# Kernel optimization log

Measured on AMD Instinct MI355X. Metric: run time of the kernel, lower is better.

Reference implementation:

```python
import jax, jax.numpy as jnp
import numpy as np
import math

D_MODEL = 1024
EXPAND = 2
D_INNER = EXPAND * D_MODEL  # 2048
D_STATE = 16
D_CONV = 4
DT_RANK = math.ceil(D_MODEL / 16)  # 64
BATCH = 1
SEQLEN = 2048


def _silu(x):
    return x * jax.nn.sigmoid(x)


def _selective_scan(u, delta, A, B, C, D, z, delta_bias):
    """u, delta, z: (b,d,l); A: (d,n); B, C: (b,n,l); D, delta_bias: (d)."""
    delta = jax.nn.softplus(delta + delta_bias[None, :, None])        # (b,d,l)
    dA = jnp.exp(jnp.einsum('bdl,dn->lbdn', delta, A))                # (l,b,d,n)
    dBu = jnp.einsum('bdl,bnl->lbdn', delta * u, B)                   # (l,b,d,n)
    Ct = jnp.transpose(C, (2, 0, 1))                                  # (l,b,n)

    def step(h, inp):
        dA_t, dBu_t, C_t = inp
        h = dA_t * h + dBu_t                                          # (b,d,n)
        y = jnp.einsum('bdn,bn->bd', h, C_t)
        return h, y

    h0 = jnp.zeros((u.shape[0], u.shape[1], A.shape[1]), dtype=u.dtype)
    _, ys = jax.lax.scan(step, h0, (dA, dBu, Ct))                     # ys: (l,b,d)
    y = jnp.transpose(ys, (1, 2, 0))                                  # (b,d,l)
    y = y + D[:, None] * u
    return y * _silu(z)


def _causal_conv1d(x, conv_w, conv_b):
    """x: (b,d,l); conv_w: (d,w); conv_b: (d). Depthwise causal conv."""
    x_pad = jnp.pad(x, ((0, 0), (0, 0), (D_CONV - 1, 0)))
    kernel = conv_w[:, None, :]  # (d, 1, w)
    y = jax.lax.conv_general_dilated(
        x_pad, kernel, window_strides=(1,), padding='VALID',
        dimension_numbers=('NCH', 'OIH', 'NCH'),
        feature_group_count=D_INNER)
    return y + conv_b[None, :, None]


def setup_inputs() -> dict:
    key = jax.random.key(0)
    ks = jax.random.split(key, 12)
    hidden_states = jax.random.normal(ks[0], (BATCH, SEQLEN, D_MODEL), dtype=jnp.float32)
    in_proj_w = jax.random.normal(ks[1], (2 * D_INNER, D_MODEL), dtype=jnp.float32) * (D_MODEL ** -0.5)
    conv_w = jax.random.normal(ks[2], (D_INNER, D_CONV), dtype=jnp.float32) * (D_CONV ** -0.5)
    conv_b = jnp.zeros((D_INNER,), dtype=jnp.float32)
    dt_std = DT_RANK ** -0.5

    def dt_bias(k):
        dt = jnp.exp(jax.random.uniform(k, (D_INNER,)) * (math.log(0.1) - math.log(0.001)) + math.log(0.001))
        dt = jnp.clip(dt, 1e-4, None)
        return dt + jnp.log(-jnp.expm1(-dt))  # inverse softplus

    A_log = jnp.log(jnp.broadcast_to(jnp.arange(1, D_STATE + 1, dtype=jnp.float32), (D_INNER, D_STATE)))
    x1_proj_w = jax.random.normal(ks[3], (DT_RANK + 2 * D_STATE, D_INNER), dtype=jnp.float32) * (D_INNER ** -0.5)
    dt1_proj_w = jax.random.uniform(ks[4], (D_INNER, DT_RANK), minval=-dt_std, maxval=dt_std)
    dt1_proj_b = dt_bias(ks[5])
    x2_proj_w = jax.random.normal(ks[6], (DT_RANK + 2 * D_STATE, D_INNER), dtype=jnp.float32) * (D_INNER ** -0.5)
    dt2_proj_w = jax.random.uniform(ks[7], (D_INNER, DT_RANK), minval=-dt_std, maxval=dt_std)
    dt2_proj_b = dt_bias(ks[8])
    out_proj_w = jax.random.normal(ks[9], (D_MODEL, D_INNER), dtype=jnp.float32) * (D_INNER ** -0.5)
    return {
        'hidden_states': hidden_states,
        'in_proj_w': in_proj_w, 'conv_w': conv_w, 'conv_b': conv_b,
        'x1_proj_w': x1_proj_w, 'dt1_proj_w': dt1_proj_w, 'dt1_proj_b': dt1_proj_b,
        'A1_log': A_log, 'D1': jnp.ones((D_INNER,), dtype=jnp.float32),
        'x2_proj_w': x2_proj_w, 'dt2_proj_w': dt2_proj_w, 'dt2_proj_b': dt2_proj_b,
        'A2_log': A_log, 'D2': jnp.ones((D_INNER,), dtype=jnp.float32),
        'out_proj_w': out_proj_w,
    }


def reference(hidden_states, in_proj_w, conv_w, conv_b,
              x1_proj_w, dt1_proj_w, dt1_proj_b, A1_log, D1,
              x2_proj_w, dt2_proj_w, dt2_proj_b, A2_log, D2,
              out_proj_w):
    # in_proj: (b,l,d) @ W^T -> (b, 2*d_inner, l)
    xz = jnp.einsum('bld,ed->bel', hidden_states, in_proj_w)
    x, z = jnp.split(xz, 2, axis=1)                                   # (b,d_inner,l) each
    A1 = -jnp.exp(A1_log.astype(jnp.float32))
    A2 = -jnp.exp(A2_log.astype(jnp.float32))
    x = _silu(_causal_conv1d(x, conv_w, conv_b))                      # (b,d_inner,l)

    def branch_params(xp_w, dtp_w):
        dbl = jnp.einsum('bdl,kd->bkl', x, xp_w)                      # (b, r+2n, l)
        dt, Bm, Cm = jnp.split(dbl, [DT_RANK, DT_RANK + D_STATE], axis=1)
        dt = jnp.einsum('brl,dr->bdl', dt, dtp_w)
        return dt, Bm, Cm

    dt1, B1, C1 = branch_params(x1_proj_w, dt1_proj_w)
    dt2, B2, C2 = branch_params(x2_proj_w, dt2_proj_w)
    y1 = _selective_scan(x, dt1, A1, B1, C1, D1.astype(jnp.float32), z, dt1_proj_b.astype(jnp.float32))
    y2 = _selective_scan(x, dt2, A2, B2, C2, D2.astype(jnp.float32), z, dt2_proj_b.astype(jnp.float32))
    y = y1 - y2                                                       # (b,d_inner,l)
    out = jnp.einsum('bdl,od->blo', y, out_proj_w)                    # (b,l,d_model)
    return out
```

## Files before the change

### kernel.cpp

```cpp
#include <hip/hip_runtime.h>
#include <math.h>

#define SEQ 2048
#define DMODEL 1024
#define DIN 2048
#define NST 16
#define DTR 64
#define CH 32
#define NCH (SEQ / CH)
#define LOG2E 1.4426950408889634f

typedef __attribute__((ext_vector_type(8))) _Float16 f16x8;
typedef __attribute__((ext_vector_type(4))) float f32x4;

__device__ __forceinline__ ushort f2h(float f) {
  union { _Float16 h; ushort u; } c; c.h = (_Float16)f; return c.u;
}
__device__ __forceinline__ float h2f(ushort u) {
  union { ushort u; _Float16 h; } c; c.u = u; return (float)c.h;
}
__device__ __forceinline__ ushort2 split2(float v) {
  ushort hh = f2h(v);
  return make_ushort2(hh, f2h((v - h2f(hh)) * 2048.f));
}
__device__ __forceinline__ float join2(ushort2 p) {
  return h2f(p.x) + h2f(p.y) * (1.f / 2048.f);
}
__device__ __forceinline__ float splus(float v) {
  return v > 20.f ? v : log1pf(__expf(v));
}
__device__ __forceinline__ void powers16(float e, float* p) {
  float e2 = e * e, e4 = e2 * e2, e8 = e4 * e4;
  p[0] = e;       p[1] = e2;       p[2] = e2 * e;   p[3] = e4;
  p[4] = e4 * e;  p[5] = e4 * e2;  p[6] = e4 * p[2]; p[7] = e8;
  p[8] = e8 * e;  p[9] = e8 * e2;  p[10] = e8 * p[2]; p[11] = e8 * e4;
  p[12] = e8 * p[4]; p[13] = e8 * p[5]; p[14] = e8 * p[6]; p[15] = e8 * e8;
}

#define GLL(g, l) __builtin_amdgcn_global_load_lds( \
    (const __attribute__((address_space(1))) void*)(g), \
    (__attribute__((address_space(3))) void*)(l), 16, 0, 0)

#define XCD_SWZ(BMv, BNv)                                              \
  const int nwg_ = gridDim.x * gridDim.y;                              \
  const int flat_ = blockIdx.y * gridDim.x + blockIdx.x;               \
  const int swz_ = (flat_ & 7) * (nwg_ >> 3) + (flat_ >> 3);           \
  const int m0 = (swz_ / gridDim.x) * (BMv);                           \
  const int n0 = (swz_ % gridDim.x) * (BNv);

template<int BM, int BN, int SPLITK, int MODE>
__global__ __launch_bounds__(256, 2) void gemm3p(const ushort* __restrict__ Ahi,
                                                 const ushort* __restrict__ Alo,
                                                 const ushort* __restrict__ Bhi,
                                                 const ushort* __restrict__ Blo,
                                                 float* __restrict__ C,
                                                 int M, int N, int K) {
  constexpr int WM = BM / 2, WN = BN / 2, TM = WM / 16, TN = WN / 16;
  constexpr int SA = BM / 16, SB = BN / 16;
  constexpr bool dropB = (MODE == 2);
  __shared__ __align__(16) ushort sAh[2][BM * 32], sAl[2][BM * 32];
  __shared__ __align__(16) ushort sBh[2][BN * 32];
  __shared__ __align__(16) ushort sBl[2][dropB ? 16 : BN * 32];
  const int tid = threadIdx.x, wid = tid >> 6, lane = tid & 63;
  XCD_SWZ(BM, BN)
  const int Kc = K / SPLITK, kbeg = blockIdx.z * Kc;
  const int wm0 = (wid >> 1) * WM, wn0 = (wid & 1) * WN;
  const int fr = lane & 15;
  const int lrow = lane >> 2;
  const int lkc = (lane & 3) ^ ((lane >> 3) & 3);
  const int fpo = fr * 32 + (((lane >> 4) ^ ((lane >> 1) & 3)) * 8);

  f32x4 acc[TM][TN], accL[TM][TN];
#pragma unroll
  for (int mi = 0; mi < TM; ++mi)
#pragma unroll
    for (int ni = 0; ni < TN; ++ni)
#pragma unroll
      for (int r = 0; r < 4; ++r) { acc[mi][ni][r] = 0.f; accL[mi][ni][r] = 0.f; }

  for (int k0 = 0; k0 < Kc; k0 += 64) {
    __syncthreads();
#pragma unroll
    for (int kk = 0; kk < 2; ++kk) {
      const int kg = kbeg + k0 + kk * 32 + lkc * 8;
#pragma unroll
      for (int i = 0; i < SA / 4; ++i) {
        const int seg = wid * (SA / 4) + i;
        const size_t ga = (size_t)(m0 + seg * 16 + lrow) * K + kg;
        GLL(&Ahi[ga], &sAh[kk][seg * 512]);
        GLL(&Alo[ga], &sAl[kk][seg * 512]);
      }
#pragma unroll
      for (int i = 0; i < SB / 4; ++i) {
        const int seg = wid * (SB / 4) + i;
        const size_t ga = (size_t)(n0 + seg * 16 + lrow) * K + kg;
        GLL(&Bhi[ga], &sBh[kk][seg * 512]);
        if constexpr (!dropB) GLL(&Blo[ga], &sBl[kk][seg * 512]);
      }
    }
    __syncthreads();

#pragma unroll
    for (int kk = 0; kk < 2; ++kk) {
      f16x8 ah[TM], al[TM], bh[TN], bl[TN];
#pragma unroll
      for (int mi = 0; mi < TM; ++mi) {
        const int r = (wm0 / 16 + mi) * 512 + fpo;
        ah[mi] = *(const f16x8*)&sAh[kk][r];
        al[mi] = *(const f16x8*)&sAl[kk][r];
      }
#pragma unroll
      for (int ni = 0; ni < TN; ++ni) {
        const int r = (wn0 / 16 + ni) * 512 + fpo;
        bh[ni] = *(const f16x8*)&sBh[kk][r];
        if constexpr (!dropB) bl[ni] = *(const f16x8*)&sBl[kk][r];
      }
#pragma unroll
      for (int mi = 0; mi < TM; ++mi)
#pragma unroll
        for (int ni = 0; ni < TN; ++ni) {
          acc[mi][ni] = __builtin_amdgcn_mfma_f32_16x16x32_f16(ah[mi], bh[ni], acc[mi][ni], 0, 0, 0);
          accL[mi][ni] = __builtin_amdgcn_mfma_f32_16x16x32_f16(al[mi], bh[ni], accL[mi][ni], 0, 0, 0);
          if constexpr (!dropB)
            accL[mi][ni] = __builtin_amdgcn_mfma_f32_16x16x32_f16(ah[mi], bl[ni], accL[mi][ni], 0, 0, 0);
        }
    }
  }

  float* __restrict__ Co = C + (size_t)blockIdx.z * M * N;
#pragma unroll
  for (int mi = 0; mi < TM; ++mi)
#pragma unroll
    for (int ni = 0; ni < TN; ++ni)
#pragma unroll
      for (int r = 0; r < 4; ++r)
        Co[(size_t)(m0 + wm0 + mi * 16 + (lane >> 4) * 4 + r) * N + n0 + wn0 + ni * 16 + fr] =
            acc[mi][ni][r] + accL[mi][ni][r] * (1.f / 2048.f);
}

__global__ __launch_bounds__(256, 2) void dt_mfma(const ushort* __restrict__ dtT_hi,
                                                  const ushort* __restrict__ dtT_lo,
                                                  const ushort* __restrict__ dw_hi,
                                                  const ushort* __restrict__ dw_lo,
                                                  const float* __restrict__ b1,
                                                  const float* __restrict__ b2,
                                                  ushort2* __restrict__ sp1,
                                                  ushort2* __restrict__ sp2) {
  const int br = blockIdx.z;
  const ushort* __restrict__ Ah = dtT_hi + (size_t)br * 131072;
  const ushort* __restrict__ Al_ = dtT_lo + (size_t)br * 131072;
  const ushort* __restrict__ Bh = dw_hi + (size_t)br * 131072;
  const ushort* __restrict__ Bl = dw_lo + (size_t)br * 131072;
  const float* __restrict__ bias = br ? b2 : b1;
  ushort2* __restrict__ o = br ? sp2 : sp1;
  __shared__ __align__(16) ushort sAh[2][4096], sAl[2][4096];
  __shared__ __align__(16) ushort sBh[2][4096], sBl[2][4096];
  const int tid = threadIdx.x, wid = tid >> 6, lane = tid & 63;
  XCD_SWZ(128, 128)
  const int wm0 = (wid >> 1) * 64, wn0 = (wid & 1) * 64;
  const int fr = lane & 15;
  const int lrow = lane >> 2;
  const int lkc = (lane & 3) ^ ((lane >> 3) & 3);
  const int fpo = fr * 32 + (((lane >> 4) ^ ((lane >> 1) & 3)) * 8);

  f32x4 acc[4][4], accL[4][4];
#pragma unroll
  for (int mi = 0; mi < 4; ++mi)
#pragma unroll
    for (int ni = 0; ni < 4; ++ni)
#pragma unroll
      for (int r = 0; r < 4; ++r) { acc[mi][ni][r] = 0.f; accL[mi][ni][r] = 0.f; }

#pragma unroll
  for (int kk = 0; kk < 2; ++kk) {
    const int kg = kk * 32 + lkc * 8;
#pragma unroll
    for (int i = 0; i < 2; ++i) {
      const int seg = wid * 2 + i;
      const size_t ga = (size_t)(m0 + seg * 16 + lrow) * 64 + kg;
      GLL(&Ah[ga], &sAh[kk][seg * 512]);
      GLL(&Al_[ga], &sAl[kk][seg * 512]);
      const size_t gb = (size_t)(n0 + seg * 16 + lrow) * 64 + kg;
      GLL(&Bh[gb], &sBh[kk][seg * 512]);
      GLL(&Bl[gb], &sBl[kk][seg * 512]);
    }
  }
  __syncthreads();

#pragma unroll
  for (int kk = 0; kk < 2; ++kk) {
    f16x8 ah[4], al[4], bh[4], bl[4];
#pragma unroll
    for (int mi = 0; mi < 4; ++mi) {
      const int r = (wm0 / 16 + mi) * 512 + fpo;
      ah[mi] = *(const f16x8*)&sAh[kk][r];
      al[mi] = *(const f16x8*)&sAl[kk][r];
    }
#pragma unroll
    for (int ni = 0; ni < 4; ++ni) {
      const int r = (wn0 / 16 + ni) * 512 + fpo;
      bh[ni] = *(const f16x8*)&sBh[kk][r];
      bl[ni] = *(const f16x8*)&sBl[kk][r];
    }
#pragma unroll
    for (int mi = 0; mi < 4; ++mi)
#pragma unroll
      for (int ni = 0; ni < 4; ++ni) {
        acc[mi][ni] = __builtin_amdgcn_mfma_f32_16x16x32_f16(ah[mi], bh[ni], acc[mi][ni], 0, 0, 0);
        accL[mi][ni] = __builtin_amdgcn_mfma_f32_16x16x32_f16(al[mi], bh[ni], accL[mi][ni], 0, 0, 0);
        accL[mi][ni] = __builtin_amdgcn_mfma_f32_16x16x32_f16(ah[mi], bl[ni], accL[mi][ni], 0, 0, 0);
      }
  }

#pragma unroll
  for (int ni = 0; ni < 4; ++ni) {
    const int n = n0 + wn0 + ni * 16 + fr;
    const float bv = bias[n];
#pragma unroll
    for (int mi = 0; mi < 4; ++mi)
#pragma unroll
      for (int r = 0; r < 4; ++r) {
        const int m = m0 + wm0 + mi * 16 + (lane >> 4) * 4 + r;
        const float v = splus(acc[mi][ni][r] + accL[mi][ni][r] * (1.f / 2048.f) + bv);
        o[(size_t)m * DIN + n] = split2(v);
      }
  }
}

__device__ __forceinline__ void split_store4h(float4 v, ushort* hi, ushort* lo, size_t i) {
  ushort h0 = f2h(v.x), h1 = f2h(v.y), h2 = f2h(v.z), h3 = f2h(v.w);
  *(ushort4*)&hi[i] = make_ushort4(h0, h1, h2, h3);
  *(ushort4*)&lo[i] = make_ushort4(f2h((v.x - h2f(h0)) * 2048.f), f2h((v.y - h2f(h1)) * 2048.f),
                                   f2h((v.z - h2f(h2)) * 2048.f), f2h((v.w - h2f(h3)) * 2048.f));
}

__global__ __launch_bounds__(256) void cvt_fused(const float* __restrict__ inw,
                                                 const float* __restrict__ hid,
                                                 const float* __restrict__ x1w,
                                                 const float* __restrict__ x2w,
                                                 const float* __restrict__ dtw1,
                                                 const float* __restrict__ dtw2,
                                                 ushort* __restrict__ w_hi, ushort* __restrict__ w_lo,
                                                 ushort* __restrict__ h_hi,
                                                 ushort* __restrict__ wx_hi, ushort* __restrict__ wx_lo,
                                                 ushort* __restrict__ dw_hi, ushort* __restrict__ dw_lo) {
  const int q = blockIdx.x * 256 + threadIdx.x;
  if (q >= 1048576 && q < 1572864) {
    const size_t i = (size_t)(q - 1048576) * 4;
    float4 v = *(const float4*)&hid[i];
    *(ushort4*)&h_hi[i] = make_ushort4(f2h(v.x), f2h(v.y), f2h(v.z), f2h(v.w));
    return;
  }
  const float* src; ushort* dhi; ushort* dlo; int base;
  if (q < 1048576)       { src = inw; dhi = w_hi;  dlo = w_lo;  base = q; }
  else if (q < 1622016)  { src = x1w; dhi = wx_hi; dlo = wx_lo; base = q - 1572864; }
  else if (q < 1671168)  { src = x2w; dhi = wx_hi + 196608; dlo = wx_lo + 196608; base = q - 1622016; }
  else if (q < 1703936)  { src = dtw1; dhi = dw_hi; dlo = dw_lo; base = q - 1671168; }
  else                   { src = dtw2; dhi = dw_hi + 131072; dlo = dw_lo + 131072; base = q - 1703936; }
  const size_t i = (size_t)base * 4;
  split_store4h(*(const float4*)&src[i], dhi, dlo, i);
}

__global__ __launch_bounds__(256) void reduce_out(const float* __restrict__ p,
                                                  float* __restrict__ o, int n) {
  const int i = (blockIdx.x * 256 + threadIdx.x) * 4;
  if (i >= n) return;
  float4 a = *(const float4*)&p[i];
  float4 b = *(const float4*)&p[(size_t)n + i];
  float4 c = *(const float4*)&p[(size_t)2 * n + i];
  float4 d = *(const float4*)&p[(size_t)3 * n + i];
  *(float4*)&o[i] = make_float4(a.x + b.x + c.x + d.x, a.y + b.y + c.y + d.y,
                                a.z + b.z + c.z + d.z, a.w + b.w + c.w + d.w);
}

__global__ __launch_bounds__(256) void conv_tr_kernel(const float* __restrict__ xz,
                                                      const float* __restrict__ cw,
                                                      const float* __restrict__ cb,
                                                      ushort* __restrict__ xcT_hi,
                                                      ushort* __restrict__ xcT_lo,
                                                      ushort2* __restrict__ zs) {
  const int l0 = blockIdx.x * 64, d0 = blockIdx.y * 64;
  const int tid = threadIdx.x;
  __shared__ float xin[64][68];
  __shared__ float To[64][65];
  __shared__ float cwS[64][4];
  __shared__ float cbS[64];

  for (int i = tid; i < 1024; i += 256) {
    const int d = i >> 4, q = i & 15;
    float4 v = *(const float4*)&xz[(size_t)(d0 + d) * SEQ + l0 + q * 4];
    xin[d][3 + q * 4 + 0] = v.x; xin[d][3 + q * 4 + 1] = v.y;
    xin[d][3 + q * 4 + 2] = v.z; xin[d][3 + q * 4 + 3] = v.w;
  }
  if (tid < 192) {
    const int j = tid >> 6, d = tid & 63;
    const int l = l0 - 3 + j;
    xin[d][j] = (l >= 0) ? xz[(size_t)(d0 + d) * SEQ + l] : 0.f;
  }
  if (tid < 64) {
    cbS[tid] = cb[d0 + tid];
    float4 w = *(const float4*)&cw[(d0 + tid) * 4];
    cwS[tid][0] = w.x; cwS[tid][1] = w.y; cwS[tid][2] = w.z; cwS[tid][3] = w.w;
  }
  __syncthreads();

  for (int i = tid; i < 4096; i += 256) {
    const int d = i >> 6, l = i & 63;
    float a = cbS[d] + cwS[d][0] * xin[d][l] + cwS[d][1] * xin[d][l + 1] +
              cwS[d][2] * xin[d][l + 2] + cwS[d][3] * xin[d][l + 3];
    To[d][l] = a / (1.f + __expf(-a));
  }
  __syncthreads();

  for (int i = tid; i < 4096; i += 256) {
    const int l = i >> 6, dd = i & 63;
    float v = To[dd][l];
    ushort h = f2h(v);
    xcT_hi[(size_t)(l0 + l) * DIN + d0 + dd] = h;
    xcT_lo[(size_t)(l0 + l) * DIN + d0 + dd] = f2h((v - h2f(h)) * 2048.f);
  }
  __syncthreads();

  for (int i = tid; i < 1024; i += 256) {
    const int d = i >> 4, q = i & 15;
    float4 v = *(const float4*)&xz[(size_t)(DIN + d0 + d) * SEQ + l0 + q * 4];
    To[d][q * 4 + 0] = v.x / (1.f + __expf(-v.x));
    To[d][q * 4 + 1] = v.y / (1.f + __expf(-v.y));
    To[d][q * 4 + 2] = v.z / (1.f + __expf(-v.z));
    To[d][q * 4 + 3] = v.w / (1.f + __expf(-v.w));
  }
  __syncthreads();
  for (int i = tid; i < 4096; i += 256) {
    const int l = i >> 6, dd = i & 63;
    zs[(size_t)(l0 + l) * DIN + d0 + dd] = split2(To[dd][l]);
  }
}

__global__ __launch_bounds__(256) void reduce_dblT_kernel(const float* __restrict__ p,
                                                          float* __restrict__ BT1,
                                                          float* __restrict__ CT1,
                                                          float* __restrict__ BT2,
                                                          float* __restrict__ CT2,
                                                          ushort* __restrict__ dtT_hi,
                                                          ushort* __restrict__ dtT_lo) {
  const int NE = SEQ * 192;
  const int idx = blockIdx.x * 256 + threadIdx.x;
  float s = 0.f;
#pragma unroll
  for (int cc = 0; cc < 16; ++cc) s += p[(size_t)cc * NE + idx];
  const int l = idx / 192, k = idx - l * 192;
  if (k < 64) {
    const size_t off = (size_t)l * 64 + k;
    const ushort hh = f2h(s);
    dtT_hi[off] = hh; dtT_lo[off] = f2h((s - h2f(hh)) * 2048.f);
  } else if (k < 80)  BT1[l * NST + (k - 64)] = s;
  else if (k < 96)    CT1[l * NST + (k - 80)] = s;
  else if (k < 160) {
    const size_t off = 131072 + (size_t)l * 64 + (k - 96);
    const ushort hh = f2h(s);
    dtT_hi[off] = hh; dtT_lo[off] = f2h((s - h2f(hh)) * 2048.f);
  }
  else if (k < 176)   BT2[l * NST + (k - 160)] = s;
  else                CT2[l * NST + (k - 176)] = s;
}

__global__ __launch_bounds__(256) void scan_phase_a(const ushort* __restrict__ uhi,
                                                    const ushort* __restrict__ ulo,
                                                    const ushort2* __restrict__ sp1,
                                                    const ushort2* __restrict__ sp2,
                                                    const float* __restrict__ BT1,
                                                    const float* __restrict__ BT2,
                                                    const float* __restrict__ Al1,
                                                    const float* __restrict__ Al2,
                                                    float* __restrict__ hend,
                                                    float* __restrict__ Pend) {
  const int c = blockIdx.y, t0 = c * CH;
  const int d = blockIdx.x * 256 + threadIdx.x;
  const size_t gbase = (size_t)t0 * DIN + d;

  __shared__ __align__(16) float Bs[2][CH][NST];
  {
    const int j = threadIdx.x;
    if (j < 128) ((float4*)&Bs[0][0][0])[j] = ((const float4*)&BT1[(size_t)t0 * NST])[j];
    else ((float4*)&Bs[1][0][0])[j - 128] = ((const float4*)&BT2[(size_t)t0 * NST])[j - 128];
  }
  __syncthreads();

  bool fast = true;
#pragma unroll
  for (int n = 0; n < NST; ++n) {
    float k1 = __expf(Al1[(size_t)d * NST + n]);
    float k2 = __expf(Al2[(size_t)d * NST + n]);
    fast = fast && (fabsf(k1 - (float)(n + 1)) < 1e-3f) && (fabsf(k2 - (float)(n + 1)) < 1e-3f);
  }
  float h1[NST], h2[NST];
#pragma unroll
  for (int n = 0; n < NST; ++n) { h1[n] = 0.f; h2[n] = 0.f; }
  float S1 = 0.f, S2 = 0.f;

  if (fast) {
    for (int tt = 0; tt < CH / 4; ++tt) {
      float s1[4], s2[4], ua[4];
#pragma unroll
      for (int j = 0; j < 4; ++j) {
        const size_t idx = gbase + (size_t)(tt * 4 + j) * DIN;
        s1[j] = join2(sp1[idx]);
        s2[j] = join2(sp2[idx]);
        ua[j] = h2f(uhi[idx]) + h2f(ulo[idx]) * (1.f / 2048.f);
      }
#pragma unroll
      for (int j = 0; j < 4; ++j) {
        const int t = tt * 4 + j;
        S1 += s1[j]; S2 += s2[j];
        const float spu1 = s1[j] * ua[j], spu2 = s2[j] * ua[j];
        float p[NST];
        powers16(__expf(-s1[j]), p);
#pragma unroll
        for (int n = 0; n < NST; ++n) h1[n] = fmaf(p[n], h1[n], spu1 * Bs[0][t][n]);
        powers16(__expf(-s2[j]), p);
#pragma unroll
        for (int n = 0; n < NST; ++n) h2[n] = fmaf(p[n], h2[n], spu2 * Bs[1][t][n]);
      }
    }
  } else {
    float A1e[NST], A2e[NST];
#pragma unroll
    for (int n = 0; n < NST; ++n) {
      A1e[n] = -__expf(Al1[(size_t)d * NST + n]) * LOG2E;
      A2e[n] = -__expf(Al2[(size_t)d * NST + n]) * LOG2E;
    }
    for (int tt = 0; tt < CH / 4; ++tt) {
      float s1[4], s2[4], ua[4];
#pragma unroll
      for (int j = 0; j < 4; ++j) {
        const size_t idx = gbase + (size_t)(tt * 4 + j) * DIN;
        s1[j] = join2(sp1[idx]);
        s2[j] = join2(sp2[idx]);
        ua[j] = h2f(uhi[idx]) + h2f(ulo[idx]) * (1.f / 2048.f);
      }
#pragma unroll
      for (int j = 0; j < 4; ++j) {
        const int t = tt * 4 + j;
        S1 += s1[j]; S2 += s2[j];
        const float spu1 = s1[j] * ua[j], spu2 = s2[j] * ua[j];
#pragma unroll
        for (int n = 0; n < NST; ++n) {
          h1[n] = fmaf(exp2f(A1e[n] * s1[j]), h1[n], spu1 * Bs[0][t][n]);
          h2[n] = fmaf(exp2f(A2e[n] * s2[j]), h2[n], spu2 * Bs[1][t][n]);
        }
      }
    }
  }

  float P1[NST], P2[NST];
  if (fast) {
    powers16(__expf(-S1), P1);
    powers16(__expf(-S2), P2);
  } else {
#pragma unroll
    for (int n = 0; n < NST; ++n) {
      P1[n] = exp2f(-__expf(Al1[(size_t)d * NST + n]) * LOG2E * S1);
      P2[n] = exp2f(-__expf(Al2[(size_t)d * NST + n]) * LOG2E * S2);
    }
  }
  const size_t b1 = ((size_t)c * DIN + d) * NST;
  const size_t b2 = ((size_t)(NCH + c) * DIN + d) * NST;
#pragma unroll
  for (int n = 0; n < NST; n += 4) {
    *(float4*)&hend[b1 + n] = make_float4(h1[n], h1[n + 1], h1[n + 2], h1[n + 3]);
    *(float4*)&Pend[b1 + n] = make_float4(P1[n], P1[n + 1], P1[n + 2], P1[n + 3]);
    *(float4*)&hend[b2 + n] = make_float4(h2[n], h2[n + 1], h2[n + 2], h2[n + 3]);
    *(float4*)&Pend[b2 + n] = make_float4(P2[n], P2[n + 1], P2[n + 2], P2[n + 3]);
  }
}

__global__ __launch_bounds__(256) void carry_cvt(const float* __restrict__ hend,
                                                 float* __restrict__ PendHin,
                                                 const float* __restrict__ outw,
                                                 ushort* __restrict__ ow_hi) {
  const int b = blockIdx.x;
  if (b < 256) {
    const int flat = b * 256 + threadIdx.x;
    const int br = flat >> 15;
    const int dn = flat & 32767;
    float h = 0.f;
    for (int c = 0; c < NCH; ++c) {
      size_t idx = ((size_t)(br * NCH + c) << 15) + dn;
      float Pv = PendHin[idx];
      float he = hend[idx];
      PendHin[idx] = h;
      h = fmaf(Pv, h, he);
    }
  } else {
    const size_t i = ((size_t)(b - 256) * 256 + threadIdx.x) * 4;
    float4 v = *(const float4*)&outw[i];
    *(ushort4*)&ow_hi[i] = make_ushort4(f2h(v.x), f2h(v.y), f2h(v.z), f2h(v.w));
  }
}

__global__ __launch_bounds__(256) void scan_phase_c(const ushort* __restrict__ uhi,
                                                    const ushort* __restrict__ ulo,
                                                    const ushort2* __restrict__ sp1,
                                                    const ushort2* __restrict__ sp2,
                                                    const float* __restrict__ BT1,
                                                    const float* __restrict__ CT1,
                                                    const float* __restrict__ BT2,
                                                    const float* __restrict__ CT2,
                                                    const float* __restrict__ Al1,
                                                    const float* __restrict__ Al2,
                                                    const float* __restrict__ D1,
                                                    const float* __restrict__ D2,
                                                    const float* __restrict__ hin,
                                                    const ushort2* __restrict__ zs,
                                                    ushort* __restrict__ yd_hi,
                                                    ushort* __restrict__ yd_lo) {
  const int c = blockIdx.y, t0 = c * CH;
  const int d = blockIdx.x * 256 + threadIdx.x;
  const size_t gbase = (size_t)t0 * DIN + d;

  __shared__ __align__(16) float Bs[2][CH][NST];
  __shared__ __align__(16) float Cs[2][CH][NST];
  {
    const int j = threadIdx.x;
    if (j < 128) {
      ((float4*)&Bs[0][0][0])[j] = ((const float4*)&BT1[(size_t)t0 * NST])[j];
      ((float4*)&Cs[0][0][0])[j] = ((const float4*)&CT1[(size_t)t0 * NST])[j];
    } else {
      ((float4*)&Bs[1][0][0])[j - 128] = ((const float4*)&BT2[(size_t)t0 * NST])[j - 128];
      ((float4*)&Cs[1][0][0])[j - 128] = ((const float4*)&CT2[(size_t)t0 * NST])[j - 128];
    }
  }
  __syncthreads();

  bool fast = true;
#pragma unroll
  for (int n = 0; n < NST; ++n) {
    float k1 = __expf(Al1[(size_t)d * NST + n]);
    float k2 = __expf(Al2[(size_t)d * NST + n]);
    fast = fast && (fabsf(k1 - (float)(n + 1)) < 1e-3f) && (fabsf(k2 - (float)(n + 1)) < 1e-3f);
  }
  const float Ddd = D1[d] - D2[d];
  float h1[NST], h2[NST];
  const size_t hb1 = ((size_t)c * DIN + d) * NST;
  const size_t hb2 = ((size_t)(NCH + c) * DIN + d) * NST;
#pragma unroll
  for (int n = 0; n < NST; n += 4) {
    float4 v1 = *(const float4*)&hin[hb1 + n];
    h1[n] = v1.x; h1[n + 1] = v1.y; h1[n + 2] = v1.z; h1[n + 3] = v1.w;
    float4 v2 = *(const float4*)&hin[hb2 + n];
    h2[n] = v2.x; h2[n + 1] = v2.y; h2[n + 2] = v2.z; h2[n + 3] = v2.w;
  }

  if (fast) {
    for (int tt = 0; tt < CH / 4; ++tt) {
      float s1[4], s2[4], ua[4];
#pragma unroll
      for (int j = 0; j < 4; ++j) {
        const size_t idx = gbase + (size_t)(tt * 4 + j) * DIN;
        s1[j] = join2(sp1[idx]);
        s2[j] = join2(sp2[idx]);
        ua[j] = h2f(uhi[idx]) + h2f(ulo[idx]) * (1.f / 2048.f);
      }
#pragma unroll
      for (int j = 0; j < 4; ++j) {
        const int t = tt * 4 + j;
        const size_t idx = gbase + (size_t)t * DIN;
        const float spu1 = s1[j] * ua[j], spu2 = s2[j] * ua[j];
        float p[NST];
        float y1 = 0.f, y2 = 0.f;
        powers16(__expf(-s1[j]), p);
#pragma unroll
        for (int n = 0; n < NST; ++n) {
          h1[n] = fmaf(p[n], h1[n], spu1 * Bs[0][t][n]);
          y1 = fmaf(h1[n], Cs[0][t][n], y1);
        }
        powers16(__expf(-s2[j]), p);
#pragma unroll
        for (int n = 0; n < NST; ++n) {
          h2[n] = fmaf(p[n], h2[n], spu2 * Bs[1][t][n]);
          y2 = fmaf(h2[n], Cs[1][t][n], y2);
        }
        const float zv = join2(zs[idx]);
        const float yd = (y1 - y2 + Ddd * ua[j]) * zv;
        const ushort hh = f2h(yd);
        yd_hi[idx] = hh;
        yd_lo[idx] = f2h((yd - h2f(hh)) * 2048.f);
      }
    }
  } else {
    float A1e[NST], A2e[NST];
#pragma unroll
    for (int n = 0; n < NST; ++n) {
      A1e[n] = -__expf(Al1[(size_t)d * NST + n]) * LOG2E;
      A2e[n] = -__expf(Al2[(size_t)d * NST + n]) * LOG2E;
    }
    for (int tt = 0; tt < CH / 4; ++tt) {
      float s1[4], s2[4], ua[4];
#pragma unroll
      for (int j = 0; j < 4; ++j) {
        const size_t idx = gbase + (size_t)(tt * 4 + j) * DIN;
        s1[j] = join2(sp1[idx]);
        s2[j] = join2(sp2[idx]);
        ua[j] = h2f(uhi[idx]) + h2f(ulo[idx]) * (1.f / 2048.f);
      }
#pragma unroll
      for (int j = 0; j < 4; ++j) {
        const int t = tt * 4 + j;
        const size_t idx = gbase + (size_t)t * DIN;
        const float spu1 = s1[j] * ua[j], spu2 = s2[j] * ua[j];
        float y1 = 0.f, y2 = 0.f;
#pragma unroll
        for (int n = 0; n < NST; ++n) {
          h1[n] = fmaf(exp2f(A1e[n] * s1[j]), h1[n], spu1 * Bs[0][t][n]);
          y1 = fmaf(h1[n], Cs[0][t][n], y1);
          h2[n] = fmaf(exp2f(A2e[n] * s2[j]), h2[n], spu2 * Bs[1][t][n]);
          y2 = fmaf(h2[n], Cs[1][t][n], y2);
        }
        const float zv = join2(zs[idx]);
        const float yd = (y1 - y2 + Ddd * ua[j]) * zv;
        const ushort hh = f2h(yd);
        yd_hi[idx] = hh;
        yd_lo[idx] = f2h((yd - h2f(hh)) * 2048.f);
      }
    }
  }
}

extern "C" void kernel_launch(void* const* d_in, const int* in_sizes, int n_in,
                              void* d_out, int out_size, void* d_ws, size_t ws_size,
                              hipStream_t stream) {
  const float* hidden = (const float*)d_in[0];
  const float* in_proj_w = (const float*)d_in[1];
  const float* conv_w = (const float*)d_in[2];
  const float* conv_b = (const float*)d_in[3];
  const float* x1w = (const float*)d_in[4];
  const float* dtw1 = (const float*)d_in[5];
  const float* dtb1 = (const float*)d_in[6];
  const float* Al1 = (const float*)d_in[7];
  const float* D1 = (const float*)d_in[8];
  const float* x2w = (const float*)d_in[9];
  const float* dtw2 = (const float*)d_in[10];
  const float* dtb2 = (const float*)d_in[11];
  const float* Al2 = (const float*)d_in[12];
  const float* D2 = (const float*)d_in[13];
  const float* outw = (const float*)d_in[14];
  float* out = (float*)d_out;

  float* ws = (float*)d_ws;
  float* xz = ws;
  float* xcTbuf = xz + (size_t)4096 * SEQ;
  float* dtTbuf = xcTbuf + (size_t)SEQ * DIN;
  float* spbuf1 = dtTbuf + (size_t)192 * SEQ;
  float* spbuf2 = spbuf1 + (size_t)SEQ * DIN;
  float* zsbuf = spbuf2 + (size_t)SEQ * DIN;
  float* hendB = zsbuf + (size_t)SEQ * DIN;
  float* PendB = hendB + (size_t)2 * NCH * DIN * NST;
  float* BT1 = PendB + (size_t)2 * NCH * DIN * NST;
  float* CT1 = BT1 + (size_t)SEQ * NST;
  float* BT2 = CT1 + (size_t)SEQ * NST;
  float* CT2 = BT2 + (size_t)SEQ * NST;
  float* wxp = CT2 + (size_t)SEQ * NST;

  ushort* xcT_hi = (ushort*)xcTbuf;
  ushort* xcT_lo = (ushort*)(xcTbuf + 2097152);
  ushort* dtT_hi = (ushort*)dtTbuf;
  ushort* dtT_lo = dtT_hi + 262144;
  ushort2* sp1 = (ushort2*)spbuf1;
  ushort2* sp2 = (ushort2*)spbuf2;
  ushort2* zs = (ushort2*)zsbuf;
  ushort* w_hi = (ushort*)zsbuf;
  ushort* w_lo = (ushort*)(zsbuf + 2097152);
  ushort* h_hi = (ushort*)hendB;
  ushort* dw_hi = ((ushort*)hendB) + 2097152;
  ushort* dw_lo = dw_hi + 262144;
  ushort* wx_hi = (ushort*)wxp;
  ushort* wx_lo = (ushort*)(wxp + 196608);
  float* xp_part = spbuf1;
  ushort* yd_hi = (ushort*)xcTbuf;
  ushort* yd_lo = (ushort*)(xcTbuf + 2097152);
  ushort* ow_hi = (ushort*)xz;
  float* opart = spbuf1;
  dim3 blk(256);

  cvt_fused<<<dim3(6784), blk, 0, stream>>>(in_proj_w, hidden, x1w, x2w, dtw1, dtw2,
                                            w_hi, w_lo, h_hi, wx_hi, wx_lo, dw_hi, dw_lo);

  gemm3p<128, 128, 1, 2><<<dim3(SEQ / 128, 4096 / 128, 1), blk, 0, stream>>>(
      w_hi, w_lo, h_hi, h_hi, xz, 4096, SEQ, DMODEL);

  conv_tr_kernel<<<dim3(SEQ / 64, DIN / 64), blk, 0, stream>>>(
      xz, conv_w, conv_b, xcT_hi, xcT_lo, zs);

  gemm3p<128, 64, 16, 0><<<dim3(192 / 64, SEQ / 128, 16), blk, 0, stream>>>(
      xcT_hi, xcT_lo, wx_hi, wx_lo, xp_part, SEQ, 192, DIN);

  reduce_dblT_kernel<<<dim3(192 * SEQ / 256), blk, 0, stream>>>(
      xp_part, BT1, CT1, BT2, CT2, dtT_hi, dtT_lo);

  dt_mfma<<<dim3(DIN / 128, SEQ / 128, 2), blk, 0, stream>>>(
      dtT_hi, dtT_lo, dw_hi, dw_lo, dtb1, dtb2, sp1, sp2);

  scan_phase_a<<<dim3(DIN / 256, NCH), blk, 0, stream>>>(
      xcT_hi, xcT_lo, sp1, sp2, BT1, BT2, Al1, Al2, hendB, PendB);
  carry_cvt<<<dim3(2304), blk, 0, stream>>>(hendB, PendB, outw, ow_hi);
  scan_phase_c<<<dim3(DIN / 256, NCH), blk, 0, stream>>>(
      xcT_hi, xcT_lo, sp1, sp2, BT1, CT1, BT2, CT2, Al1, Al2,
      D1, D2, PendB, zs, yd_hi, yd_lo);

  gemm3p<128, 128, 4, 2><<<dim3(DMODEL / 128, SEQ / 128, 4), blk, 0, stream>>>(
      yd_hi, yd_lo, ow_hi, ow_hi, opart, SEQ, DMODEL, DIN);
  reduce_out<<<dim3(SEQ * DMODEL / 1024), blk, 0, stream>>>(opart, out, SEQ * DMODEL);
}
```

Measured before the change: 316.8 us.

## Double-buffer GEMM K-loop staging and prefetch carry loads in carry_cvt

```diff
diff --git a/kernel.cpp b/kernel.cpp
--- a/kernel.cpp
+++ b/kernel.cpp
@@ -55,12 +55,13 @@
                                                  const ushort* __restrict__ Blo,
                                                  float* __restrict__ C,
                                                  int M, int N, int K) {
+  constexpr int BK = 32;
   constexpr int WM = BM / 2, WN = BN / 2, TM = WM / 16, TN = WN / 16;
   constexpr int SA = BM / 16, SB = BN / 16;
   constexpr bool dropB = (MODE == 2);
-  __shared__ __align__(16) ushort sAh[2][BM * 32], sAl[2][BM * 32];
-  __shared__ __align__(16) ushort sBh[2][BN * 32];
-  __shared__ __align__(16) ushort sBl[2][dropB ? 16 : BN * 32];
+  __shared__ __align__(16) ushort sAh[2][BM * BK], sAl[2][BM * BK];
+  __shared__ __align__(16) ushort sBh[2][BN * BK];
+  __shared__ __align__(16) ushort sBl[2][dropB ? 16 : BN * BK];
   const int tid = threadIdx.x, wid = tid >> 6, lane = tid & 63;
   XCD_SWZ(BM, BN)
   const int Kc = K / SPLITK, kbeg = blockIdx.z * Kc;
@@ -78,54 +79,61 @@
 #pragma unroll
       for (int r = 0; r < 4; ++r) { acc[mi][ni][r] = 0.f; accL[mi][ni][r] = 0.f; }
 
-  for (int k0 = 0; k0 < Kc; k0 += 64) {
+#define STG(BUF, K0) do {                                                  \
+    const int kg_ = kbeg + (K0) + lkc * 8;                                 \
+    _Pragma("unroll")                                                      \
+    for (int i_ = 0; i_ < SA / 4; ++i_) {                                  \
+      const int seg_ = wid * (SA / 4) + i_;                                \
+      const size_t ga_ = (size_t)(m0 + seg_ * 16 + lrow) * K + kg_;        \
+      GLL(&Ahi[ga_], &sAh[BUF][seg_ * 512]);                               \
+      GLL(&Alo[ga_], &sAl[BUF][seg_ * 512]);                               \
+    }                                                                      \
+    _Pragma("unroll")                                                      \
+    for (int i_ = 0; i_ < SB / 4; ++i_) {                                  \
+      const int seg_ = wid * (SB / 4) + i_;                                \
+      const size_t gb_ = (size_t)(n0 + seg_ * 16 + lrow) * K + kg_;        \
+      GLL(&Bhi[gb_], &sBh[BUF][seg_ * 512]);                               \
+      if constexpr (!dropB) GLL(&Blo[gb_], &sBl[BUF][seg_ * 512]);         \
+    }                                                                      \
+  } while (0)
+
+#define CMP(BUF) do {                                                      \
+    f16x8 ah_[TM], al_[TM], bh_[TN], bl_[TN];                              \
+    _Pragma("unroll")                                                      \
+    for (int mi = 0; mi < TM; ++mi) {                                      \
+      const int r_ = (wm0 / 16 + mi) * 512 + fpo;                          \
+      ah_[mi] = *(const f16x8*)&sAh[BUF][r_];                              \
+      al_[mi] = *(const f16x8*)&sAl[BUF][r_];                              \
+    }                                                                      \
+    _Pragma("unroll")                                                      \
+    for (int ni = 0; ni < TN; ++ni) {                                      \
+      const int r_ = (wn0 / 16 + ni) * 512 + fpo;                          \
+      bh_[ni] = *(const f16x8*)&sBh[BUF][r_];                              \
+      if constexpr (!dropB) bl_[ni] = *(const f16x8*)&sBl[BUF][r_];        \
+    }                                                                      \
+    _Pragma("unroll")                                                      \
+    for (int mi = 0; mi < TM; ++mi)                                        \
+      _Pragma("unroll")                                                    \
+      for (int ni = 0; ni < TN; ++ni) {                                    \
+        acc[mi][ni] = __builtin_amdgcn_mfma_f32_16x16x32_f16(ah_[mi], bh_[ni], acc[mi][ni], 0, 0, 0);   \
+        accL[mi][ni] = __builtin_amdgcn_mfma_f32_16x16x32_f16(al_[mi], bh_[ni], accL[mi][ni], 0, 0, 0); \
+        if constexpr (!dropB)                                              \
+          accL[mi][ni] = __builtin_amdgcn_mfma_f32_16x16x32_f16(ah_[mi], bl_[ni], accL[mi][ni], 0, 0, 0); \
+      }                                                                    \
+  } while (0)
+
+  STG(0, 0);
+  __syncthreads();
+  for (int k0 = 0; k0 < Kc; k0 += 2 * BK) {
+    if (k0 + BK < Kc) STG(1, k0 + BK);
+    CMP(0);
     __syncthreads();
-#pragma unroll
-    for (int kk = 0; kk < 2; ++kk) {
-      const int kg = kbeg + k0 + kk * 32 + lkc * 8;
-#pragma unroll
-      for (int i = 0; i < SA / 4; ++i) {
-        const int seg = wid * (SA / 4) + i;
-        const size_t ga = (size_t)(m0 + seg * 16 + lrow) * K + kg;
-        GLL(&Ahi[ga], &sAh[kk][seg * 512]);
-        GLL(&Alo[ga], &sAl[kk][seg * 512]);
-      }
-#pragma unroll
-      for (int i = 0; i < SB / 4; ++i) {
-        const int seg = wid * (SB / 4) + i;
-        const size_t ga = (size_t)(n0 + seg * 16 + lrow) * K + kg;
-        GLL(&Bhi[ga], &sBh[kk][seg * 512]);
-        if constexpr (!dropB) GLL(&Blo[ga], &sBl[kk][seg * 512]);
-      }
-    }
+    if (k0 + 2 * BK < Kc) STG(0, k0 + 2 * BK);
+    if (k0 + BK < Kc) CMP(1);
     __syncthreads();
-
-#pragma unroll
-    for (int kk = 0; kk < 2; ++kk) {
-      f16x8 ah[TM], al[TM], bh[TN], bl[TN];
-#pragma unroll
-      for (int mi = 0; mi < TM; ++mi) {
-        const int r = (wm0 / 16 + mi) * 512 + fpo;
-        ah[mi] = *(const f16x8*)&sAh[kk][r];
-        al[mi] = *(const f16x8*)&sAl[kk][r];
-      }
-#pragma unroll
-      for (int ni = 0; ni < TN; ++ni) {
-        const int r = (wn0 / 16 + ni) * 512 + fpo;
-        bh[ni] = *(const f16x8*)&sBh[kk][r];
-        if constexpr (!dropB) bl[ni] = *(const f16x8*)&sBl[kk][r];
-      }
-#pragma unroll
-      for (int mi = 0; mi < TM; ++mi)
-#pragma unroll
-        for (int ni = 0; ni < TN; ++ni) {
-          acc[mi][ni] = __builtin_amdgcn_mfma_f32_16x16x32_f16(ah[mi], bh[ni], acc[mi][ni], 0, 0, 0);
-          accL[mi][ni] = __builtin_amdgcn_mfma_f32_16x16x32_f16(al[mi], bh[ni], accL[mi][ni], 0, 0, 0);
-          if constexpr (!dropB)
-            accL[mi][ni] = __builtin_amdgcn_mfma_f32_16x16x32_f16(ah[mi], bl[ni], accL[mi][ni], 0, 0, 0);
-        }
-    }
-  }
+  }
+#undef STG
+#undef CMP
 
   float* __restrict__ Co = C + (size_t)blockIdx.z * M * N;
 #pragma unroll
@@ -483,13 +491,17 @@
     const int flat = b * 256 + threadIdx.x;
     const int br = flat >> 15;
     const int dn = flat & 32767;
+    size_t idx = ((size_t)(br * NCH) << 15) + dn;
     float h = 0.f;
+    float Pv = PendHin[idx];
+    float he = hend[idx];
     for (int c = 0; c < NCH; ++c) {
-      size_t idx = ((size_t)(br * NCH + c) << 15) + dn;
-      float Pv = PendHin[idx];
-      float he = hend[idx];
+      const size_t nidx = idx + (1u << 15);
+      float Pn = 0.f, hn = 0.f;
+      if (c + 1 < NCH) { Pn = PendHin[nidx]; hn = hend[nidx]; }
       PendHin[idx] = h;
       h = fmaf(Pv, h, he);
+      Pv = Pn; he = hn; idx = nidx;
     }
   } else {
     const size_t i = ((size_t)(b - 256) * 256 + threadIdx.x) * 4;
```

Result: slower. 324.5 us (+2.4%).

## Fuse dt projection and softplus into both scan phases via per-block MFMA tiles

Applied to the files above, without the earlier changes.

```diff
diff --git a/kernel.cpp b/kernel.cpp
--- a/kernel.cpp
+++ b/kernel.cpp
@@ -138,92 +138,64 @@
             acc[mi][ni][r] + accL[mi][ni][r] * (1.f / 2048.f);
 }
 
-__global__ __launch_bounds__(256, 2) void dt_mfma(const ushort* __restrict__ dtT_hi,
-                                                  const ushort* __restrict__ dtT_lo,
-                                                  const ushort* __restrict__ dw_hi,
-                                                  const ushort* __restrict__ dw_lo,
-                                                  const float* __restrict__ b1,
-                                                  const float* __restrict__ b2,
-                                                  ushort2* __restrict__ sp1,
-                                                  ushort2* __restrict__ sp2) {
-  const int br = blockIdx.z;
-  const ushort* __restrict__ Ah = dtT_hi + (size_t)br * 131072;
-  const ushort* __restrict__ Al_ = dtT_lo + (size_t)br * 131072;
-  const ushort* __restrict__ Bh = dw_hi + (size_t)br * 131072;
-  const ushort* __restrict__ Bl = dw_lo + (size_t)br * 131072;
-  const float* __restrict__ bias = br ? b2 : b1;
-  ushort2* __restrict__ o = br ? sp2 : sp1;
-  __shared__ __align__(16) ushort sAh[2][4096], sAl[2][4096];
-  __shared__ __align__(16) ushort sBh[2][4096], sBl[2][4096];
-  const int tid = threadIdx.x, wid = tid >> 6, lane = tid & 63;
-  XCD_SWZ(128, 128)
-  const int wm0 = (wid >> 1) * 64, wn0 = (wid & 1) * 64;
-  const int fr = lane & 15;
-  const int lrow = lane >> 2;
-  const int lkc = (lane & 3) ^ ((lane >> 3) & 3);
-  const int fpo = fr * 32 + (((lane >> 4) ^ ((lane >> 1) & 3)) * 8);
-
-  f32x4 acc[4][4], accL[4][4];
-#pragma unroll
-  for (int mi = 0; mi < 4; ++mi)
-#pragma unroll
-    for (int ni = 0; ni < 4; ++ni)
-#pragma unroll
-      for (int r = 0; r < 4; ++r) { acc[mi][ni][r] = 0.f; accL[mi][ni][r] = 0.f; }
-
-#pragma unroll
-  for (int kk = 0; kk < 2; ++kk) {
-    const int kg = kk * 32 + lkc * 8;
-#pragma unroll
-    for (int i = 0; i < 2; ++i) {
-      const int seg = wid * 2 + i;
-      const size_t ga = (size_t)(m0 + seg * 16 + lrow) * 64 + kg;
-      GLL(&Ah[ga], &sAh[kk][seg * 512]);
-      GLL(&Al_[ga], &sAl[kk][seg * 512]);
-      const size_t gb = (size_t)(n0 + seg * 16 + lrow) * 64 + kg;
-      GLL(&Bh[gb], &sBh[kk][seg * 512]);
-      GLL(&Bl[gb], &sBl[kk][seg * 512]);
-    }
-  }
-  __syncthreads();
-
-#pragma unroll
-  for (int kk = 0; kk < 2; ++kk) {
-    f16x8 ah[4], al[4], bh[4], bl[4];
-#pragma unroll
-    for (int mi = 0; mi < 4; ++mi) {
-      const int r = (wm0 / 16 + mi) * 512 + fpo;
-      ah[mi] = *(const f16x8*)&sAh[kk][r];
-      al[mi] = *(const f16x8*)&sAl[kk][r];
+__device__ __forceinline__ void dt_tile(const ushort* __restrict__ dtT_hi,
+                                        const ushort* __restrict__ dtT_lo,
+                                        const ushort* __restrict__ dw_hi,
+                                        const ushort* __restrict__ dw_lo,
+                                        const float* __restrict__ b1,
+                                        const float* __restrict__ b2,
+                                        int t0, int d0, int tid,
+                                        float (*sp_s)[CH][260]) {
+  const int wid = tid >> 6, lane = tid & 63;
+  const int fr = lane & 15, kq = lane >> 4;
+#pragma unroll
+  for (int br = 0; br < 2; ++br) {
+    const ushort* __restrict__ Ah = dtT_hi + br * 131072;
+    const ushort* __restrict__ Al = dtT_lo + br * 131072;
+    const ushort* __restrict__ Bh = dw_hi + br * 131072;
+    const ushort* __restrict__ Bl = dw_lo + br * 131072;
+    const float* __restrict__ bias = br ? b2 : b1;
+    f32x4 acc[2][4], accL[2][4];
+#pragma unroll
+    for (int mi = 0; mi < 2; ++mi)
+#pragma unroll
+      for (int ni = 0; ni < 4; ++ni)
+#pragma unroll
+        for (int r = 0; r < 4; ++r) { acc[mi][ni][r] = 0.f; accL[mi][ni][r] = 0.f; }
+#pragma unroll
+    for (int kk = 0; kk < 2; ++kk) {
+      f16x8 a_h[2], a_l[2], b_h[4], b_l[4];
+#pragma unroll
+      for (int mi = 0; mi < 2; ++mi) {
+        const size_t off = (size_t)(t0 + mi * 16 + fr) * 64 + kk * 32 + kq * 8;
+        a_h[mi] = *(const f16x8*)&Ah[off];
+        a_l[mi] = *(const f16x8*)&Al[off];
+      }
+#pragma unroll
+      for (int ni = 0; ni < 4; ++ni) {
+        const size_t off = (size_t)(d0 + wid * 64 + ni * 16 + fr) * 64 + kk * 32 + kq * 8;
+        b_h[ni] = *(const f16x8*)&Bh[off];
+        b_l[ni] = *(const f16x8*)&Bl[off];
+      }
+#pragma unroll
+      for (int mi = 0; mi < 2; ++mi)
+#pragma unroll
+        for (int ni = 0; ni < 4; ++ni) {
+          acc[mi][ni] = __builtin_amdgcn_mfma_f32_16x16x32_f16(a_h[mi], b_h[ni], acc[mi][ni], 0, 0, 0);
+          accL[mi][ni] = __builtin_amdgcn_mfma_f32_16x16x32_f16(a_l[mi], b_h[ni], accL[mi][ni], 0, 0, 0);
+          accL[mi][ni] = __builtin_amdgcn_mfma_f32_16x16x32_f16(a_h[mi], b_l[ni], accL[mi][ni], 0, 0, 0);
+        }
     }
 #pragma unroll
     for (int ni = 0; ni < 4; ++ni) {
-      const int r = (wn0 / 16 + ni) * 512 + fpo;
-      bh[ni] = *(const f16x8*)&sBh[kk][r];
-      bl[ni] = *(const f16x8*)&sBl[kk][r];
-    }
-#pragma unroll
-    for (int mi = 0; mi < 4; ++mi)
-#pragma unroll
-      for (int ni = 0; ni < 4; ++ni) {
-        acc[mi][ni] = __builtin_amdgcn_mfma_f32_16x16x32_f16(ah[mi], bh[ni], acc[mi][ni], 0, 0, 0);
-        accL[mi][ni] = __builtin_amdgcn_mfma_f32_16x16x32_f16(al[mi], bh[ni], accL[mi][ni], 0, 0, 0);
-        accL[mi][ni] = __builtin_amdgcn_mfma_f32_16x16x32_f16(ah[mi], bl[ni], accL[mi][ni], 0, 0, 0);
-      }
-  }
-
-#pragma unroll
-  for (int ni = 0; ni < 4; ++ni) {
-    const int n = n0 + wn0 + ni * 16 + fr;
-    const float bv = bias[n];
-#pragma unroll
-    for (int mi = 0; mi < 4; ++mi)
-#pragma unroll
-      for (int r = 0; r < 4; ++r) {
-        const int m = m0 + wm0 + mi * 16 + (lane >> 4) * 4 + r;
-        const float v = splus(acc[mi][ni][r] + accL[mi][ni][r] * (1.f / 2048.f) + bv);
-        o[(size_t)m * DIN + n] = split2(v);
-      }
+      const float bv = bias[d0 + wid * 64 + ni * 16 + fr];
+#pragma unroll
+      for (int mi = 0; mi < 2; ++mi)
+#pragma unroll
+        for (int r = 0; r < 4; ++r)
+          sp_s[br][mi * 16 + kq * 4 + r][wid * 64 + ni * 16 + fr] =
+              splus(acc[mi][ni][r] + accL[mi][ni][r] * (1.f / 2048.f) + bv);
+    }
   }
 }
 
@@ -366,8 +338,12 @@
 
 __global__ __launch_bounds__(256) void scan_phase_a(const ushort* __restrict__ uhi,
                                                     const ushort* __restrict__ ulo,
-                                                    const ushort2* __restrict__ sp1,
-                                                    const ushort2* __restrict__ sp2,
+                                                    const ushort* __restrict__ dtT_hi,
+                                                    const ushort* __restrict__ dtT_lo,
+                                                    const ushort* __restrict__ dw_hi,
+                                                    const ushort* __restrict__ dw_lo,
+                                                    const float* __restrict__ dtb1,
+                                                    const float* __restrict__ dtb2,
                                                     const float* __restrict__ BT1,
                                                     const float* __restrict__ BT2,
                                                     const float* __restrict__ Al1,
@@ -375,15 +351,18 @@
                                                     float* __restrict__ hend,
                                                     float* __restrict__ Pend) {
   const int c = blockIdx.y, t0 = c * CH;
-  const int d = blockIdx.x * 256 + threadIdx.x;
+  const int d0b = blockIdx.x * 256;
+  const int d = d0b + threadIdx.x;
   const size_t gbase = (size_t)t0 * DIN + d;
 
   __shared__ __align__(16) float Bs[2][CH][NST];
+  __shared__ __align__(16) float sp_s[2][CH][260];
   {
     const int j = threadIdx.x;
     if (j < 128) ((float4*)&Bs[0][0][0])[j] = ((const float4*)&BT1[(size_t)t0 * NST])[j];
     else ((float4*)&Bs[1][0][0])[j - 128] = ((const float4*)&BT2[(size_t)t0 * NST])[j - 128];
   }
+  dt_tile(dtT_hi, dtT_lo, dw_hi, dw_lo, dtb1, dtb2, t0, d0b, threadIdx.x, sp_s);
   __syncthreads();
 
   bool fast = true;
@@ -404,8 +383,8 @@
 #pragma unroll
       for (int j = 0; j < 4; ++j) {
         const size_t idx = gbase + (size_t)(tt * 4 + j) * DIN;
-        s1[j] = join2(sp1[idx]);
-        s2[j] = join2(sp2[idx]);
+        s1[j] = sp_s[0][tt * 4 + j][threadIdx.x];
+        s2[j] = sp_s[1][tt * 4 + j][threadIdx.x];
         ua[j] = h2f(uhi[idx]) + h2f(ulo[idx]) * (1.f / 2048.f);
       }
 #pragma unroll
@@ -434,8 +413,8 @@
 #pragma unroll
       for (int j = 0; j < 4; ++j) {
         const size_t idx = gbase + (size_t)(tt * 4 + j) * DIN;
-        s1[j] = join2(sp1[idx]);
-        s2[j] = join2(sp2[idx]);
+        s1[j] = sp_s[0][tt * 4 + j][threadIdx.x];
+        s2[j] = sp_s[1][tt * 4 + j][threadIdx.x];
         ua[j] = h2f(uhi[idx]) + h2f(ulo[idx]) * (1.f / 2048.f);
       }
 #pragma unroll
@@ -500,8 +479,12 @@
 
 __global__ __launch_bounds__(256) void scan_phase_c(const ushort* __restrict__ uhi,
                                                     const ushort* __restrict__ ulo,
-                                                    const ushort2* __restrict__ sp1,
-                                                    const ushort2* __restrict__ sp2,
+                                                    const ushort* __restrict__ dtT_hi,
+                                                    const ushort* __restrict__ dtT_lo,
+                                                    const ushort* __restrict__ dw_hi,
+                                                    const ushort* __restrict__ dw_lo,
+                                                    const float* __restrict__ dtb1,
+                                                    const float* __restrict__ dtb2,
                                                     const float* __restrict__ BT1,
                                                     const float* __restrict__ CT1,
                                                     const float* __restrict__ BT2,
@@ -515,11 +498,13 @@
                                                     ushort* __restrict__ yd_hi,
                                                     ushort* __restrict__ yd_lo) {
   const int c = blockIdx.y, t0 = c * CH;
-  const int d = blockIdx.x * 256 + threadIdx.x;
+  const int d0b = blockIdx.x * 256;
+  const int d = d0b + threadIdx.x;
   const size_t gbase = (size_t)t0 * DIN + d;
 
   __shared__ __align__(16) float Bs[2][CH][NST];
   __shared__ __align__(16) float Cs[2][CH][NST];
+  __shared__ __align__(16) float sp_s[2][CH][260];
   {
     const int j = threadIdx.x;
     if (j < 128) {
@@ -530,6 +515,7 @@
       ((float4*)&Cs[1][0][0])[j - 128] = ((const float4*)&CT2[(size_t)t0 * NST])[j - 128];
     }
   }
+  dt_tile(dtT_hi, dtT_lo, dw_hi, dw_lo, dtb1, dtb2, t0, d0b, threadIdx.x, sp_s);
   __syncthreads();
 
   bool fast = true;
@@ -557,8 +543,8 @@
 #pragma unroll
       for (int j = 0; j < 4; ++j) {
         const size_t idx = gbase + (size_t)(tt * 4 + j) * DIN;
-        s1[j] = join2(sp1[idx]);
-        s2[j] = join2(sp2[idx]);
+        s1[j] = sp_s[0][tt * 4 + j][threadIdx.x];
+        s2[j] = sp_s[1][tt * 4 + j][threadIdx.x];
         ua[j] = h2f(uhi[idx]) + h2f(ulo[idx]) * (1.f / 2048.f);
       }
 #pragma unroll
@@ -599,8 +585,8 @@
 #pragma unroll
       for (int j = 0; j < 4; ++j) {
         const size_t idx = gbase + (size_t)(tt * 4 + j) * DIN;
-        s1[j] = join2(sp1[idx]);
-        s2[j] = join2(sp2[idx]);
+        s1[j] = sp_s[0][tt * 4 + j][threadIdx.x];
+        s2[j] = sp_s[1][tt * 4 + j][threadIdx.x];
         ua[j] = h2f(uhi[idx]) + h2f(ulo[idx]) * (1.f / 2048.f);
       }
 #pragma unroll
@@ -665,13 +651,11 @@
   ushort* xcT_lo = (ushort*)(xcTbuf + 2097152);
   ushort* dtT_hi = (ushort*)dtTbuf;
   ushort* dtT_lo = dtT_hi + 262144;
-  ushort2* sp1 = (ushort2*)spbuf1;
-  ushort2* sp2 = (ushort2*)spbuf2;
   ushort2* zs = (ushort2*)zsbuf;
   ushort* w_hi = (ushort*)zsbuf;
   ushort* w_lo = (ushort*)(zsbuf + 2097152);
   ushort* h_hi = (ushort*)hendB;
-  ushort* dw_hi = ((ushort*)hendB) + 2097152;
+  ushort* dw_hi = (ushort*)(spbuf2 + 3932160);
   ushort* dw_lo = dw_hi + 262144;
   ushort* wx_hi = (ushort*)wxp;
   ushort* wx_lo = (ushort*)(wxp + 196608);
@@ -680,6 +664,7 @@
   ushort* yd_lo = (ushort*)(xcTbuf + 2097152);
   ushort* ow_hi = (ushort*)xz;
   float* opart = spbuf1;
+
   dim3 blk(256);
 
   cvt_fused<<<dim3(6784), blk, 0, stream>>>(in_proj_w, hidden, x1w, x2w, dtw1, dtw2,
@@ -697,15 +682,13 @@
   reduce_dblT_kernel<<<dim3(192 * SEQ / 256), blk, 0, stream>>>(
       xp_part, BT1, CT1, BT2, CT2, dtT_hi, dtT_lo);
 
-  dt_mfma<<<dim3(DIN / 128, SEQ / 128, 2), blk, 0, stream>>>(
-      dtT_hi, dtT_lo, dw_hi, dw_lo, dtb1, dtb2, sp1, sp2);
-
   scan_phase_a<<<dim3(DIN / 256, NCH), blk, 0, stream>>>(
-      xcT_hi, xcT_lo, sp1, sp2, BT1, BT2, Al1, Al2, hendB, PendB);
+      xcT_hi, xcT_lo, dtT_hi, dtT_lo, dw_hi, dw_lo, dtb1, dtb2,
+      BT1, BT2, Al1, Al2, hendB, PendB);
   carry_cvt<<<dim3(2304), blk, 0, stream>>>(hendB, PendB, outw, ow_hi);
   scan_phase_c<<<dim3(DIN / 256, NCH), blk, 0, stream>>>(
-      xcT_hi, xcT_lo, sp1, sp2, BT1, CT1, BT2, CT2, Al1, Al2,
-      D1, D2, PendB, zs, yd_hi, yd_lo);
+      xcT_hi, xcT_lo, dtT_hi, dtT_lo, dw_hi, dw_lo, dtb1, dtb2,
+      BT1, CT1, BT2, CT2, Al1, Al2, D1, D2, PendB, zs, yd_hi, yd_lo);
 
   gemm3p<128, 128, 4, 2><<<dim3(DMODEL / 128, SEQ / 128, 4), blk, 0, stream>>>(
       yd_hi, yd_lo, ow_hi, ow_hi, opart, SEQ, DMODEL, DIN);
```

After: 395.6 us. 24.9% more time.
